# Optimization experiments

Measured on AMD Instinct MI355X. Metric: run time of the kernel, lower is better.

Reference implementation:

```python
import jax, jax.numpy as jnp
import numpy as np

N_HEAD = 16

def setup_inputs() -> dict:
    key = jax.random.key(0)
    k1, k2, k3 = jax.random.split(key, 3)
    B, T, D = 2, 2048, 1024
    x = jax.random.normal(k1, (B, T, D), dtype=jnp.float32)
    sigma_qkv = float(np.sqrt(2.0 / (D + 3 * D)))
    sigma_out = float(np.sqrt(2.0 / (D + D)))
    W_qkv = jax.random.truncated_normal(k2, -3.0, 3.0, (3 * D, D), dtype=jnp.float32) * sigma_qkv
    W_out = jax.random.truncated_normal(k3, -3.0, 3.0, (D, D), dtype=jnp.float32) * sigma_out
    return {"x": x, "W_qkv": W_qkv, "W_out": W_out}


def reference(x, W_qkv, W_out):
    B, T, C = x.shape
    H = N_HEAD
    hd = C // H
    qkv = x @ W_qkv.T  # (B,T,3C)
    q, k, v = jnp.split(qkv, 3, axis=-1)
    # (B,T,C) -> (B,H,T,hd)
    q = q.reshape(B, T, H, hd).transpose(0, 2, 1, 3)
    k = k.reshape(B, T, H, hd).transpose(0, 2, 1, 3)
    v = v.reshape(B, T, H, hd).transpose(0, 2, 1, 3)
    scale = 1.0 / jnp.sqrt(jnp.asarray(hd, dtype=x.dtype))
    score = jnp.einsum('bhqd,bhkd->bhqk', q, k) * scale  # (B,H,T,T)
    causal = jnp.tril(jnp.ones((T, T), dtype=bool))
    score = jnp.where(causal, score, -jnp.inf)
    attn = jax.nn.softmax(score, axis=-1)
    out = jnp.einsum('bhqk,bhkd->bhqd', attn, v)  # (B,H,T,hd)
    out = out.transpose(0, 2, 1, 3).reshape(B, T, C)
    return out @ W_out.T
```

## Files before the change

### kernel.cpp

```cpp
#include <hip/hip_runtime.h>
#include <hip/hip_bf16.h>
#include <cstdint>

typedef unsigned short u16;
typedef __attribute__((ext_vector_type(8))) short bf16x8;
typedef __attribute__((ext_vector_type(4))) float f32x4;

#define T_SEQ 2048
#define NHEAD 16
#define HDIM  64
#define NB    2

__device__ __forceinline__ float bf2f(uint32_t h) { return __uint_as_float(h << 16); }
__device__ __forceinline__ u16 f2bf(float f) {
    uint32_t u = __float_as_uint(f);
    u += 0x7fffu + ((u >> 16) & 1u);
    return (u16)(u >> 16);
}

__device__ __forceinline__ void gl_lds16(const u16* g, u16* s) {
    __builtin_amdgcn_global_load_lds(
        (const __attribute__((address_space(1))) unsigned int*)g,
        (__attribute__((address_space(3))) unsigned int*)s, 16, 0, 0);
}

__global__ void detect_dtype(const uint32_t* __restrict__ x, int* __restrict__ flag) {
    __shared__ int red[4];
    int c = 0;
#pragma unroll
    for (int j = 0; j < 4; j++) {
        uint32_t v = x[threadIdx.x * 4 + j];
        uint32_t lo = v & 0xffffu;
        uint32_t e = (lo >> 7) & 0xffu;
        if (lo != 0u && e >= 110u && e <= 135u) c++;
    }
#pragma unroll
    for (int off = 32; off; off >>= 1) c += __shfl_down(c, off);
    if ((threadIdx.x & 63) == 0) red[threadIdx.x >> 6] = c;
    __syncthreads();
    if (threadIdx.x == 0)
        *flag = (red[0] + red[1] + red[2] + red[3] > 614) ? 1 : 0;
}

__global__ __launch_bounds__(256) void to_bf16(
    const void* __restrict__ src, u16* __restrict__ dst, int n4,
    const int* __restrict__ flag)
{
    int i = blockIdx.x * 256 + threadIdx.x;
    const int stride = gridDim.x * 256;
    if (*flag != 0) {
        const uint2* s = (const uint2*)src;
        uint2* d = (uint2*)dst;
        for (; i < n4; i += stride) d[i] = s[i];
    } else {
        const float4* s = (const float4*)src;
        for (; i < n4; i += stride) {
            float4 v = s[i];
            ushort4 o = { f2bf(v.x), f2bf(v.y), f2bf(v.z), f2bf(v.w) };
            *(ushort4*)(dst + (size_t)i * 4) = o;
        }
    }
}

template<int BM, int MODE>
__global__ __launch_bounds__(256, 3) void gemm_bt_mfma(
    const u16* __restrict__ A, const u16* __restrict__ B,
    int N, int K,
    u16* __restrict__ qo, u16* __restrict__ ko, u16* __restrict__ vt,
    u16* __restrict__ outb16, float* __restrict__ outf32,
    const int* __restrict__ flag)
{
    constexpr int WM = BM / 2;
    constexpr int MI = WM / 16;
    constexpr int IA = BM / 32;
    constexpr int ST = 2 * BM * 64 * 2;
    constexpr int E16 = 4 * WM * 72 * 2;
    constexpr int EF = (MODE == 1) ? 4 * WM * (WM + 4) * 4 : 0;
    constexpr int SB = (ST > E16 ? ST : E16) > EF ? (ST > E16 ? ST : E16) : EF;
    __shared__ u16 smem[SB / 2];
    u16* As = smem;
    u16* Bs = smem + BM * 64;
    const int tid = threadIdx.x;
    const int bm = blockIdx.y * BM, bn = blockIdx.x * BM;
    const int w = tid >> 6, lane = tid & 63;
    const int wm = (w >> 1) * WM, wn = (w & 1) * WM;
    const int n16 = lane & 15, quad = lane >> 4;
    const int l8 = lane >> 3, c8 = lane & 7;

    f32x4 acc[MI][MI];
#pragma unroll
    for (int mi = 0; mi < MI; mi++)
#pragma unroll
        for (int ni = 0; ni < MI; ni++) acc[mi][ni] = (f32x4){0.f, 0.f, 0.f, 0.f};

    const int KT = K >> 6;
    for (int kt = 0; kt < KT; kt++) {
        const int k0 = kt << 6;
#pragma unroll
        for (int i = 0; i < IA; i++) {
            int rowblk = (i * 4 + w) * 8;
            int row = rowblk + l8;
            int gcol = (c8 ^ l8) * 8;
            gl_lds16(A + (size_t)(bm + row) * K + k0 + gcol, As + rowblk * 64);
            gl_lds16(B + (size_t)(bn + row) * K + k0 + gcol, Bs + rowblk * 64);
        }
        __syncthreads();
#pragma unroll
        for (int ks = 0; ks < 2; ks++) {
            bf16x8 af[MI], bfr[MI];
#pragma unroll
            for (int mi = 0; mi < MI; mi++) {
                int row = wm + mi * 16 + n16;
                af[mi] = *(const bf16x8*)(As + row * 64 + (((ks * 4 + quad) ^ (n16 & 7)) * 8));
            }
#pragma unroll
            for (int ni = 0; ni < MI; ni++) {
                int row = wn + ni * 16 + n16;
                bfr[ni] = *(const bf16x8*)(Bs + row * 64 + (((ks * 4 + quad) ^ (n16 & 7)) * 8));
            }
#pragma unroll
            for (int mi = 0; mi < MI; mi++)
#pragma unroll
                for (int ni = 0; ni < MI; ni++)
                    acc[mi][ni] = __builtin_amdgcn_mfma_f32_16x16x32_bf16(
                        af[mi], bfr[ni], acc[mi][ni], 0, 0, 0);
        }
        __syncthreads();
    }

    if constexpr (MODE == 0) {
        u16* ep = smem + w * (WM * 72);
        const int which = (bn + wn) >> 10;
        const int hq = ((bn + wn) & 1023) >> 6;
        const int bb = (bm + wm) >> 11;
        const int tb = (bm + wm) & (T_SEQ - 1);
        if (which == 2) {
#pragma unroll
            for (int mi = 0; mi < MI; mi++)
#pragma unroll
                for (int ni = 0; ni < MI; ni++)
#pragma unroll
                    for (int r = 0; r < 4; r++)
                        ep[(ni * 16 + n16) * 72 + mi * 16 + quad * 4 + r] = f2bf(acc[mi][ni][r]);
            asm volatile("s_waitcnt lgkmcnt(0)" ::: "memory");
            u16* dst = vt + ((size_t)(bb * NHEAD + hq) * HDIM) * T_SEQ + tb;
#pragma unroll
            for (int it = 0; it < 8; it++) {
                int row = it * 8 + l8, col = c8 * 8;
                bf16x8 v = *(const bf16x8*)(ep + row * 72 + col);
                *(bf16x8*)(dst + (size_t)row * T_SEQ + col) = v;
            }
        } else {
            const float sc = which ? 1.f : 0.125f;
#pragma unroll
            for (int mi = 0; mi < MI; mi++)
#pragma unroll
                for (int ni = 0; ni < MI; ni++)
#pragma unroll
                    for (int r = 0; r < 4; r++)
                        ep[(mi * 16 + quad * 4 + r) * 72 + ni * 16 + n16] = f2bf(acc[mi][ni][r] * sc);
            asm volatile("s_waitcnt lgkmcnt(0)" ::: "memory");
            u16* dst = (which ? ko : qo) + ((size_t)(bb * NHEAD + hq) * T_SEQ + tb) * HDIM;
#pragma unroll
            for (int it = 0; it < 8; it++) {
                int row = it * 8 + l8, col = c8 * 8;
                bf16x8 v = *(const bf16x8*)(ep + row * 72 + col);
                *(bf16x8*)(dst + (size_t)row * HDIM + col) = v;
            }
        }
    } else {
        if (*flag == 0) {
            float* epf = (float*)smem + w * (WM * (WM + 4));
#pragma unroll
            for (int mi = 0; mi < MI; mi++)
#pragma unroll
                for (int ni = 0; ni < MI; ni++)
#pragma unroll
                    for (int r = 0; r < 4; r++)
                        epf[(mi * 16 + quad * 4 + r) * (WM + 4) + ni * 16 + n16] = acc[mi][ni][r];
            asm volatile("s_waitcnt lgkmcnt(0)" ::: "memory");
            constexpr int LPR = WM / 4;
            constexpr int RPI = 64 / LPR;
#pragma unroll
            for (int it = 0; it < WM / RPI; it++) {
                int row = it * RPI + lane / LPR, col = (lane % LPR) * 4;
                float4 v = *(const float4*)(epf + row * (WM + 4) + col);
                *(float4*)(outf32 + (size_t)(bm + wm + row) * N + bn + wn + col) = v;
            }
        } else {
            u16* ep = smem + w * (WM * 72);
#pragma unroll
            for (int mi = 0; mi < MI; mi++)
#pragma unroll
                for (int ni = 0; ni < MI; ni++)
#pragma unroll
                    for (int r = 0; r < 4; r++)
                        ep[(mi * 16 + quad * 4 + r) * 72 + ni * 16 + n16] = f2bf(acc[mi][ni][r]);
            asm volatile("s_waitcnt lgkmcnt(0)" ::: "memory");
            constexpr int LPR = WM / 8;
            constexpr int RPI = 64 / LPR;
#pragma unroll
            for (int it = 0; it < WM / RPI; it++) {
                int row = it * RPI + lane / LPR, col = (lane % LPR) * 8;
                bf16x8 v = *(const bf16x8*)(ep + row * 72 + col);
                *(bf16x8*)(outb16 + (size_t)(bm + wm + row) * N + bn + wn + col) = v;
            }
        }
    }
}

__global__ __launch_bounds__(256, 3) void attn_mfma(
    const u16* __restrict__ qb, const u16* __restrict__ kb,
    const u16* __restrict__ vt, u16* __restrict__ ob)
{
    __shared__ u16 Ks[64 * 64];
    __shared__ u16 Vs[64 * 64];
    __shared__ u16 Plds[4][2][16][72];
    const int bidx = blockIdx.x;
    const int c = bidx & 255;
    const int rr = bidx >> 8;
    const int bh = c & 31;
    const int jm = c >> 5;
    const int t = rr ? (15 - jm) : jm;
    const int w = threadIdx.x >> 6, lane = threadIdx.x & 63;
    const int n16 = lane & 15, quad = lane >> 4;
    const int l8 = lane >> 3, c8 = lane & 7;
    const size_t baseK = (size_t)bh * T_SEQ * HDIM;
    const size_t baseV = (size_t)bh * HDIM * T_SEQ;
    const int b = bh >> 4, head = bh & 15;

    bf16x8 ones;
#pragma unroll
    for (int e = 0; e < 8; e++) ones[e] = (short)0x3F80;

    auto stage = [&](int kt) {
#pragma unroll
        for (int i = 0; i < 2; i++) {
            int rowblk = w * 16 + i * 8;
            int row = rowblk + l8;
            int gc = (c8 ^ l8) * 8;
            gl_lds16(kb + baseK + (size_t)(kt * 64 + row) * HDIM + gc, Ks + rowblk * 64);
            gl_lds16(vt + baseV + (size_t)row * T_SEQ + (size_t)kt * 64 + gc, Vs + rowblk * 64);
        }
    };

    const int qrow = t * 128 + w * 32;
    bf16x8 qf[2][2];
#pragma unroll
    for (int s = 0; s < 2; s++)
#pragma unroll
        for (int ks = 0; ks < 2; ks++)
            qf[s][ks] = *(const bf16x8*)(qb + baseK +
                (size_t)(qrow + s * 16 + n16) * HDIM + ks * 32 + quad * 8);

    f32x4 accO[2][4];
#pragma unroll
    for (int s = 0; s < 2; s++)
#pragma unroll
        for (int st = 0; st < 4; st++) accO[s][st] = (f32x4){0.f, 0.f, 0.f, 0.f};
    f32x4 accL[2];
    accL[0] = (f32x4){0.f, 0.f, 0.f, 0.f};
    accL[1] = (f32x4){0.f, 0.f, 0.f, 0.f};

    const int ktmax = 2 * t + 1;
    const int kend  = 2 * t + (w >> 1);

    stage(0);
    for (int kt = 0; kt <= ktmax; kt++) {
        __syncthreads();

        const bool act = (kt <= kend);
        bf16x8 kf[2][4], vf[2][4];
        if (act) {
#pragma unroll
            for (int st = 0; st < 4; st++)
#pragma unroll
                for (int ks = 0; ks < 2; ks++) {
                    int off = (st * 16 + n16) * 64 + (((ks * 4 + quad) ^ (n16 & 7)) * 8);
                    kf[ks][st] = *(const bf16x8*)(Ks + off);
                    vf[ks][st] = *(const bf16x8*)(Vs + off);
                }
        }
        __syncthreads();

        if (kt < ktmax) stage(kt + 1);

        if (act) {
#pragma unroll
            for (int s = 0; s < 2; s++) {
                f32x4 S[4];
#pragma unroll
                for (int st = 0; st < 4; st++) S[st] = (f32x4){0.f, 0.f, 0.f, 0.f};
#pragma unroll
                for (int st = 0; st < 4; st++)
#pragma unroll
                    for (int ks = 0; ks < 2; ks++)
                        S[st] = __builtin_amdgcn_mfma_f32_16x16x32_bf16(qf[s][ks], kf[ks][st], S[st], 0, 0, 0);
                if (kt == kend) {
                    int qloc = w * 32 + s * 16 + quad * 4 - (w >> 1) * 64;
#pragma unroll
                    for (int st = 0; st < 4; st++) {
                        int kloc = st * 16 + n16;
#pragma unroll
                        for (int r = 0; r < 4; r++)
                            if (kloc > qloc + r) S[st][r] = -INFINITY;
                    }
                }
#pragma unroll
                for (int st = 0; st < 4; st++)
#pragma unroll
                    for (int r = 0; r < 4; r++) {
                        float pv = exp2f(__builtin_fmaf(S[st][r], 1.44269504f, -14.4269504f));
                        Plds[w][s][quad * 4 + r][st * 16 + n16] = (u16)(__float_as_uint(pv) >> 16);
                    }
                asm volatile("s_waitcnt lgkmcnt(0)" ::: "memory");
                bf16x8 pf[2];
#pragma unroll
                for (int ks = 0; ks < 2; ks++)
                    pf[ks] = *(const bf16x8*)(&Plds[w][s][n16][ks * 32 + quad * 8]);
#pragma unroll
                for (int st = 0; st < 4; st++)
#pragma unroll
                    for (int ks = 0; ks < 2; ks++)
                        accO[s][st] = __builtin_amdgcn_mfma_f32_16x16x32_bf16(pf[ks], vf[ks][st], accO[s][st], 0, 0, 0);
#pragma unroll
                for (int ks = 0; ks < 2; ks++)
                    accL[s] = __builtin_amdgcn_mfma_f32_16x16x32_bf16(pf[ks], ones, accL[s], 0, 0, 0);
            }
        }
    }

#pragma unroll
    for (int s = 0; s < 2; s++) {
#pragma unroll
        for (int r = 0; r < 4; r++) {
            float inv = 1.f / accL[s][r];
#pragma unroll
            for (int st = 0; st < 4; st++)
                Plds[w][s][quad * 4 + r][st * 16 + n16] = f2bf(accO[s][st][r] * inv);
        }
    }
    asm volatile("s_waitcnt lgkmcnt(0)" ::: "memory");
#pragma unroll
    for (int s = 0; s < 2; s++) {
        u16* dst = ob + ((size_t)(b * T_SEQ + qrow + s * 16)) * 1024 + head * HDIM;
#pragma unroll
        for (int it = 0; it < 2; it++) {
            int row = it * 8 + l8, col = c8 * 8;
            bf16x8 v = *(const bf16x8*)(&Plds[w][s][row][col]);
            *(bf16x8*)(dst + (size_t)row * 1024 + col) = v;
        }
    }
}

extern "C" void kernel_launch(void* const* d_in, const int* in_sizes, int n_in,
                              void* d_out, int out_size, void* d_ws, size_t ws_size,
                              hipStream_t stream) {
    const void* x    = d_in[0];
    const void* Wqkv = d_in[1];
    const void* Wout = d_in[2];

    const int Mtok = NB * T_SEQ;
    const size_t n_x    = (size_t)Mtok * 1024;
    const size_t n_wqkv = (size_t)3072 * 1024;
    const size_t n_wout = (size_t)1024 * 1024;
    const size_t qkv_elems = (size_t)NB * NHEAD * T_SEQ * HDIM;

    u16* xb    = (u16*)d_ws;
    u16* wqkvb = xb + n_x;
    u16* woutb = wqkvb + n_wqkv;
    u16* qb    = woutb + n_wout;
    u16* kb    = qb + qkv_elems;
    u16* vt    = kb + qkv_elems;
    u16* obuf  = vt + qkv_elems;
    int* flag  = (int*)(obuf + qkv_elems);

    detect_dtype<<<1, 256, 0, stream>>>((const uint32_t*)x, flag);

    to_bf16<<<1024, 256, 0, stream>>>(x,    xb,    (int)(n_x / 4),    flag);
    to_bf16<<<1024, 256, 0, stream>>>(Wqkv, wqkvb, (int)(n_wqkv / 4), flag);
    to_bf16<<<512,  256, 0, stream>>>(Wout, woutb, (int)(n_wout / 4), flag);

    gemm_bt_mfma<128, 0><<<dim3(3072 / 128, Mtok / 128), 256, 0, stream>>>(
        xb, wqkvb, 3072, 1024, qb, kb, vt, nullptr, nullptr, flag);

    attn_mfma<<<dim3(NB * NHEAD * (T_SEQ / 128)), 256, 0, stream>>>(qb, kb, vt, obuf);

    gemm_bt_mfma<64, 1><<<dim3(1024 / 64, Mtok / 64), 256, 0, stream>>>(
        obuf, woutb, 1024, 1024, nullptr, nullptr, nullptr,
        (u16*)d_out, (float*)d_out, flag);
}
```

Before: 180.9 us.

## Switch attention to 32x32 MFMA with transposed scores and register-resident P

The attention kernel now uses 32x32x16 bf16 MFMA and computes S transposed (K as the A operand, Q as B), so each lane holds a column of scores. The probabilities are converted with packed bf16 conversion and rearranged across lanes with permlane32_swap to form the A operand for the PV product. This removes the per-iteration LDS round trip for P and the waitcnt stall it required. In exchange, larger accumulators raise register pressure, which could reduce occupancy under the existing launch bounds.

Result: slower. 206.5 us (+14.1%).

```diff
diff --git a/kernel.cpp b/kernel.cpp
--- a/kernel.cpp
+++ b/kernel.cpp
@@ -5,6 +5,7 @@
 typedef unsigned short u16;
 typedef __attribute__((ext_vector_type(8))) short bf16x8;
 typedef __attribute__((ext_vector_type(4))) float f32x4;
+typedef __attribute__((ext_vector_type(16))) float f32x16;
 
 #define T_SEQ 2048
 #define NHEAD 16
@@ -16,6 +17,12 @@
     uint32_t u = __float_as_uint(f);
     u += 0x7fffu + ((u >> 16) & 1u);
     return (u16)(u >> 16);
+}
+
+__device__ __forceinline__ uint32_t cvt_pk_bf16(float lo, float hi) {
+    uint32_t r;
+    asm("v_cvt_pk_bf16_f32 %0, %1, %2" : "=v"(r) : "v"(lo), "v"(hi));
+    return r;
 }
 
 __device__ __forceinline__ void gl_lds16(const u16* g, u16* s) {
@@ -215,7 +222,7 @@
 {
     __shared__ u16 Ks[64 * 64];
     __shared__ u16 Vs[64 * 64];
-    __shared__ u16 Plds[4][2][16][72];
+    __shared__ u16 Ep[4][32][72];
     const int bidx = blockIdx.x;
     const int c = bidx & 255;
     const int rr = bidx >> 8;
@@ -223,7 +230,7 @@
     const int jm = c >> 5;
     const int t = rr ? (15 - jm) : jm;
     const int w = threadIdx.x >> 6, lane = threadIdx.x & 63;
-    const int n16 = lane & 15, quad = lane >> 4;
+    const int l31 = lane & 31, h = lane >> 5;
     const int l8 = lane >> 3, c8 = lane & 7;
     const size_t baseK = (size_t)bh * T_SEQ * HDIM;
     const size_t baseV = (size_t)bh * HDIM * T_SEQ;
@@ -245,22 +252,14 @@
     };
 
     const int qrow = t * 128 + w * 32;
-    bf16x8 qf[2][2];
-#pragma unroll
-    for (int s = 0; s < 2; s++)
-#pragma unroll
-        for (int ks = 0; ks < 2; ks++)
-            qf[s][ks] = *(const bf16x8*)(qb + baseK +
-                (size_t)(qrow + s * 16 + n16) * HDIM + ks * 32 + quad * 8);
-
-    f32x4 accO[2][4];
-#pragma unroll
-    for (int s = 0; s < 2; s++)
-#pragma unroll
-        for (int st = 0; st < 4; st++) accO[s][st] = (f32x4){0.f, 0.f, 0.f, 0.f};
-    f32x4 accL[2];
-    accL[0] = (f32x4){0.f, 0.f, 0.f, 0.f};
-    accL[1] = (f32x4){0.f, 0.f, 0.f, 0.f};
+    bf16x8 qf[4];
+#pragma unroll
+    for (int ds = 0; ds < 4; ds++)
+        qf[ds] = *(const bf16x8*)(qb + baseK + (size_t)(qrow + l31) * HDIM + ds * 16 + h * 8);
+
+    f32x16 accO0 = (f32x16)0.f;
+    f32x16 accO1 = (f32x16)0.f;
+    f32x16 accL  = (f32x16)0.f;
 
     const int ktmax = 2 * t + 1;
     const int kend  = 2 * t + (w >> 1);
@@ -270,15 +269,24 @@
         __syncthreads();
 
         const bool act = (kt <= kend);
-        bf16x8 kf[2][4], vf[2][4];
+        f32x16 S0 = (f32x16)0.f, S1 = (f32x16)0.f;
+        bf16x8 vf[2][4];
         if (act) {
 #pragma unroll
-            for (int st = 0; st < 4; st++)
-#pragma unroll
-                for (int ks = 0; ks < 2; ks++) {
-                    int off = (st * 16 + n16) * 64 + (((ks * 4 + quad) ^ (n16 & 7)) * 8);
-                    kf[ks][st] = *(const bf16x8*)(Ks + off);
-                    vf[ks][st] = *(const bf16x8*)(Vs + off);
+            for (int ds = 0; ds < 4; ds++) {
+                const int g = ds * 2 + h;
+                bf16x8 ka = *(const bf16x8*)(Ks + l31 * 64 + ((g ^ (l31 & 7)) * 8));
+                bf16x8 kc = *(const bf16x8*)(Ks + (32 + l31) * 64 + ((g ^ (l31 & 7)) * 8));
+                S0 = __builtin_amdgcn_mfma_f32_32x32x16_bf16(ka, qf[ds], S0, 0, 0, 0);
+                S1 = __builtin_amdgcn_mfma_f32_32x32x16_bf16(kc, qf[ds], S1, 0, 0, 0);
+            }
+#pragma unroll
+            for (int dblk = 0; dblk < 2; dblk++)
+#pragma unroll
+                for (int ks = 0; ks < 4; ks++) {
+                    const int row = dblk * 32 + l31;
+                    const int g = ks * 2 + h;
+                    vf[dblk][ks] = *(const bf16x8*)(Vs + row * 64 + ((g ^ (row & 7)) * 8));
                 }
         }
         __syncthreads();
@@ -286,70 +294,70 @@
         if (kt < ktmax) stage(kt + 1);
 
         if (act) {
-#pragma unroll
-            for (int s = 0; s < 2; s++) {
-                f32x4 S[4];
-#pragma unroll
-                for (int st = 0; st < 4; st++) S[st] = (f32x4){0.f, 0.f, 0.f, 0.f};
-#pragma unroll
-                for (int st = 0; st < 4; st++)
-#pragma unroll
-                    for (int ks = 0; ks < 2; ks++)
-                        S[st] = __builtin_amdgcn_mfma_f32_16x16x32_bf16(qf[s][ks], kf[ks][st], S[st], 0, 0, 0);
-                if (kt == kend) {
-                    int qloc = w * 32 + s * 16 + quad * 4 - (w >> 1) * 64;
-#pragma unroll
-                    for (int st = 0; st < 4; st++) {
-                        int kloc = st * 16 + n16;
-#pragma unroll
-                        for (int r = 0; r < 4; r++)
-                            if (kloc > qloc + r) S[st][r] = -INFINITY;
-                    }
+            if (kt == kend) {
+                const int ql = (w & 1) * 32 + l31;
+#pragma unroll
+                for (int r = 0; r < 16; r++) {
+                    const int row = (r & 3) + ((r >> 2) << 3) + 4 * h;
+                    if (row > ql)      S0[r] = -INFINITY;
+                    if (row + 32 > ql) S1[r] = -INFINITY;
                 }
-#pragma unroll
-                for (int st = 0; st < 4; st++)
-#pragma unroll
-                    for (int r = 0; r < 4; r++) {
-                        float pv = exp2f(__builtin_fmaf(S[st][r], 1.44269504f, -14.4269504f));
-                        Plds[w][s][quad * 4 + r][st * 16 + n16] = (u16)(__float_as_uint(pv) >> 16);
-                    }
-                asm volatile("s_waitcnt lgkmcnt(0)" ::: "memory");
-                bf16x8 pf[2];
-#pragma unroll
-                for (int ks = 0; ks < 2; ks++)
-                    pf[ks] = *(const bf16x8*)(&Plds[w][s][n16][ks * 32 + quad * 8]);
-#pragma unroll
-                for (int st = 0; st < 4; st++)
-#pragma unroll
-                    for (int ks = 0; ks < 2; ks++)
-                        accO[s][st] = __builtin_amdgcn_mfma_f32_16x16x32_bf16(pf[ks], vf[ks][st], accO[s][st], 0, 0, 0);
-#pragma unroll
-                for (int ks = 0; ks < 2; ks++)
-                    accL[s] = __builtin_amdgcn_mfma_f32_16x16x32_bf16(pf[ks], ones, accL[s], 0, 0, 0);
-            }
-        }
-    }
-
-#pragma unroll
-    for (int s = 0; s < 2; s++) {
-#pragma unroll
-        for (int r = 0; r < 4; r++) {
-            float inv = 1.f / accL[s][r];
-#pragma unroll
-            for (int st = 0; st < 4; st++)
-                Plds[w][s][quad * 4 + r][st * 16 + n16] = f2bf(accO[s][st][r] * inv);
-        }
+            }
+#pragma unroll
+            for (int r = 0; r < 16; r++) {
+                S0[r] = exp2f(__builtin_fmaf(S0[r], 1.44269504f, -14.4269504f));
+                S1[r] = exp2f(__builtin_fmaf(S1[r], 1.44269504f, -14.4269504f));
+            }
+            bf16x8 pf[4];
+#pragma unroll
+            for (int half = 0; half < 2; half++) {
+                {
+                    uint32_t c0 = cvt_pk_bf16(S0[half * 8 + 0], S0[half * 8 + 1]);
+                    uint32_t c1 = cvt_pk_bf16(S0[half * 8 + 2], S0[half * 8 + 3]);
+                    uint32_t c2 = cvt_pk_bf16(S0[half * 8 + 4], S0[half * 8 + 5]);
+                    uint32_t c3 = cvt_pk_bf16(S0[half * 8 + 6], S0[half * 8 + 7]);
+                    auto s0 = __builtin_amdgcn_permlane32_swap(c0, c2, false, false);
+                    auto s1 = __builtin_amdgcn_permlane32_swap(c1, c3, false, false);
+                    union { uint32_t u[4]; bf16x8 v; } uu;
+                    uu.u[0] = s0[0]; uu.u[1] = s1[0]; uu.u[2] = s0[1]; uu.u[3] = s1[1];
+                    pf[half] = uu.v;
+                }
+                {
+                    uint32_t c0 = cvt_pk_bf16(S1[half * 8 + 0], S1[half * 8 + 1]);
+                    uint32_t c1 = cvt_pk_bf16(S1[half * 8 + 2], S1[half * 8 + 3]);
+                    uint32_t c2 = cvt_pk_bf16(S1[half * 8 + 4], S1[half * 8 + 5]);
+                    uint32_t c3 = cvt_pk_bf16(S1[half * 8 + 6], S1[half * 8 + 7]);
+                    auto s0 = __builtin_amdgcn_permlane32_swap(c0, c2, false, false);
+                    auto s1 = __builtin_amdgcn_permlane32_swap(c1, c3, false, false);
+                    union { uint32_t u[4]; bf16x8 v; } uu;
+                    uu.u[0] = s0[0]; uu.u[1] = s1[0]; uu.u[2] = s0[1]; uu.u[3] = s1[1];
+                    pf[2 + half] = uu.v;
+                }
+            }
+#pragma unroll
+            for (int ks = 0; ks < 4; ks++) {
+                accL  = __builtin_amdgcn_mfma_f32_32x32x16_bf16(pf[ks], ones,       accL,  0, 0, 0);
+                accO0 = __builtin_amdgcn_mfma_f32_32x32x16_bf16(pf[ks], vf[0][ks], accO0, 0, 0, 0);
+                accO1 = __builtin_amdgcn_mfma_f32_32x32x16_bf16(pf[ks], vf[1][ks], accO1, 0, 0, 0);
+            }
+        }
+    }
+
+    u16* ep = &Ep[w][0][0];
+#pragma unroll
+    for (int r = 0; r < 16; r++) {
+        const int row = (r & 3) + ((r >> 2) << 3) + 4 * h;
+        const float inv = 1.f / accL[r];
+        ep[row * 72 + l31]      = f2bf(accO0[r] * inv);
+        ep[row * 72 + 32 + l31] = f2bf(accO1[r] * inv);
     }
     asm volatile("s_waitcnt lgkmcnt(0)" ::: "memory");
-#pragma unroll
-    for (int s = 0; s < 2; s++) {
-        u16* dst = ob + ((size_t)(b * T_SEQ + qrow + s * 16)) * 1024 + head * HDIM;
-#pragma unroll
-        for (int it = 0; it < 2; it++) {
-            int row = it * 8 + l8, col = c8 * 8;
-            bf16x8 v = *(const bf16x8*)(&Plds[w][s][row][col]);
-            *(bf16x8*)(dst + (size_t)row * 1024 + col) = v;
-        }
+    u16* dst = ob + ((size_t)(b * T_SEQ + qrow)) * 1024 + head * HDIM;
+#pragma unroll
+    for (int it = 0; it < 4; it++) {
+        int row = it * 8 + l8, col = c8 * 8;
+        bf16x8 v = *(const bf16x8*)(ep + row * 72 + col);
+        *(bf16x8*)(dst + (size_t)row * 1024 + col) = v;
     }
 }
 
```
